# Kernel tuning notes

Hardware: AMD Instinct MI355X
Metric: run time of the kernel (lower is better)

## Reference

```python
import jax, jax.numpy as jnp
import numpy as np

N_NODES = 50000
NEG_SLOPE = 0.2


def gat_conv(x, src, dst, W, a_src, a_dst, bias, heads):
    # x: [N, Fin]; W: [Fin, heads*C]; a_src/a_dst: [heads, C]; bias: [heads*C]
    n = x.shape[0]
    h = (x @ W).reshape(n, heads, -1)              # [N, H, C]
    alpha_src = jnp.einsum('nhc,hc->nh', h, a_src)  # [N, H]
    alpha_dst = jnp.einsum('nhc,hc->nh', h, a_dst)  # [N, H]
    e = alpha_src[src] + alpha_dst[dst]             # [E, H]
    e = jax.nn.leaky_relu(e, NEG_SLOPE)
    # segment softmax over edges grouped by destination node
    m = jax.ops.segment_max(e, dst, num_segments=n)          # [N, H]
    e = jnp.exp(e - jax.lax.stop_gradient(m)[dst])
    s = jax.ops.segment_sum(e, dst, num_segments=n)          # [N, H]
    alpha = e / (s[dst] + 1e-16)                              # [E, H]
    msg = h[src] * alpha[:, :, None]                          # [E, H, C]
    out = jax.ops.segment_sum(msg, dst, num_segments=n)      # [N, H, C]
    return out.reshape(n, -1) + bias


def add_self_loops(edge_index, n):
    loops = jnp.arange(n, dtype=edge_index.dtype)
    src = jnp.concatenate([edge_index[0], loops])
    dst = jnp.concatenate([edge_index[1], loops])
    return src, dst


def setup_inputs() -> dict:
    key = jax.random.key(0)
    ks = jax.random.split(key, 10)
    num_features, num_classes, heads1, c1 = 128, 40, 8, 32
    n_edges = 800000
    x = jax.random.normal(ks[0], (N_NODES, num_features), dtype=jnp.float32)
    edge_index = jax.random.randint(ks[1], (2, n_edges), 0, N_NODES, dtype=jnp.int64)
    sc = 0.1
    W1 = jax.random.normal(ks[2], (num_features, heads1 * c1), dtype=jnp.float32) * sc
    a_src1 = jax.random.normal(ks[3], (heads1, c1), dtype=jnp.float32) * sc
    a_dst1 = jax.random.normal(ks[4], (heads1, c1), dtype=jnp.float32) * sc
    b1 = jnp.zeros((heads1 * c1,), dtype=jnp.float32)
    W2 = jax.random.normal(ks[5], (heads1 * c1, num_classes), dtype=jnp.float32) * sc
    a_src2 = jax.random.normal(ks[6], (1, num_classes), dtype=jnp.float32) * sc
    a_dst2 = jax.random.normal(ks[7], (1, num_classes), dtype=jnp.float32) * sc
    b2 = jnp.zeros((num_classes,), dtype=jnp.float32)
    return {"x": x, "edge_index": edge_index, "W1": W1, "a_src1": a_src1,
            "a_dst1": a_dst1, "b1": b1, "W2": W2, "a_src2": a_src2,
            "a_dst2": a_dst2, "b2": b2}


def reference(x, edge_index, W1, a_src1, a_dst1, b1, W2, a_src2, a_dst2, b2):
    src, dst = add_self_loops(edge_index, x.shape[0])
    h = gat_conv(x, src, dst, W1, a_src1, a_dst1, b1, heads=8)
    h = jax.nn.elu(h)
    h = gat_conv(h, src, dst, W2, a_src2, a_dst2, b2, heads=1)
    return jax.nn.log_softmax(h, axis=1)
```

## Files before the change

### kernel.cpp

```cpp
#include <hip/hip_runtime.h>
#include <math.h>

#define NNODES 50000
#define F_IN   128
#define F1     256
#define H1N    8
#define NCLS   40
#define NEG    0.2f
#define MNEG  -3.0e38f
#define SCAN_BLOCKS 196
#define ACAP   64

typedef unsigned int uint32;
typedef __attribute__((ext_vector_type(8))) short short8v;
typedef __attribute__((ext_vector_type(4))) float f32x4;

__device__ __forceinline__ float leaky(float x) { return x > 0.f ? x : NEG * x; }

__device__ __forceinline__ unsigned short f2bf(float f) {
  uint32 u = __float_as_uint(f);
  u = (u + 0x7FFFu + ((u >> 16) & 1u)) >> 16;
  return (unsigned short)u;
}
__device__ __forceinline__ float bf_lo(uint32 u) { return __uint_as_float(u << 16); }
__device__ __forceinline__ float bf_hi(uint32 u) { return __uint_as_float(u & 0xFFFF0000u); }
__device__ __forceinline__ float bfu(unsigned short u) {
  return __uint_as_float((uint32)u << 16);
}

__global__ __launch_bounds__(256) void convx_k(const float* __restrict__ x,
                                               unsigned short* __restrict__ xb) {
  int i = blockIdx.x * 256 + threadIdx.x;
  float4 v = ((const float4*)x)[i];
  uint2 o;
  o.x = (uint32)f2bf(v.x) | ((uint32)f2bf(v.y) << 16);
  o.y = (uint32)f2bf(v.z) | ((uint32)f2bf(v.w) << 16);
  ((uint2*)xb)[i] = o;
}

__global__ __launch_bounds__(256) void convw_k(const float* __restrict__ W,
                                               unsigned short* __restrict__ Wt) {
  int id = blockIdx.x * 256 + threadIdx.x;
  int k = id >> 8, c = id & 255;
  Wt[c * 128 + k] = f2bf(W[id]);
}

__global__ __launch_bounds__(256) void convw2_k(const float* __restrict__ W2,
                                                unsigned short* __restrict__ Wt2) {
  int id = blockIdx.x * 256 + threadIdx.x;
  int c = id >> 8, k = id & 255;
  Wt2[c * 256 + k] = (c < NCLS) ? f2bf(W2[k * NCLS + c]) : (unsigned short)0;
}

__global__ __launch_bounds__(256) void gemm1_mfma_k(
    const unsigned short* __restrict__ xb, const unsigned short* __restrict__ Wt,
    const float* __restrict__ asrc, const float* __restrict__ adst,
    unsigned short* __restrict__ h1b, float* __restrict__ as1,
    float* __restrict__ ad1) {
  const int lane = threadIdx.x & 63;
  const int wv   = threadIdx.x >> 6;
  const int row0 = blockIdx.x * 64 + wv * 16;
  if (row0 >= NNODES) return;
  const int lrow = lane & 15;
  const int kgrp = lane >> 4;

  const short8v* xp = (const short8v*)xb;
  short8v a[4];
  #pragma unroll
  for (int ks = 0; ks < 4; ++ks)
    a[ks] = xp[(row0 + lrow) * 16 + ks * 4 + kgrp];

  const short8v* wp = (const short8v*)Wt;
  float ps[4] = {0.f, 0.f, 0.f, 0.f};
  float pd[4] = {0.f, 0.f, 0.f, 0.f};

  for (int n = 0; n < 16; ++n) {
    f32x4 acc = {0.f, 0.f, 0.f, 0.f};
    #pragma unroll
    for (int ks = 0; ks < 4; ++ks) {
      short8v b = wp[(n * 16 + lrow) * 16 + ks * 4 + kgrp];
      acc = __builtin_amdgcn_mfma_f32_16x16x32_bf16(a[ks], b, acc, 0, 0, 0);
    }
    const int col = n * 16 + lrow;
    const float ascv = asrc[col];
    const float advv = adst[col];
    #pragma unroll
    for (int r = 0; r < 4; ++r) {
      int row = row0 + kgrp * 4 + r;
      h1b[(long)row * F1 + col] = f2bf(acc[r]);
      ps[r] = fmaf(acc[r], ascv, ps[r]);
      pd[r] = fmaf(acc[r], advv, pd[r]);
    }
    if (n & 1) {
      const int head = n >> 1;
      #pragma unroll
      for (int r = 0; r < 4; ++r) {
        #pragma unroll
        for (int mask = 1; mask <= 8; mask <<= 1) {
          ps[r] += __shfl_xor(ps[r], mask, 64);
          pd[r] += __shfl_xor(pd[r], mask, 64);
        }
      }
      if (lrow == 0) {
        #pragma unroll
        for (int r = 0; r < 4; ++r) {
          int row = row0 + kgrp * 4 + r;
          as1[row * H1N + head] = ps[r];
          ad1[row * H1N + head] = pd[r];
        }
      }
      #pragma unroll
      for (int r = 0; r < 4; ++r) { ps[r] = 0.f; pd[r] = 0.f; }
    }
  }
}

__global__ __launch_bounds__(256) void hist_k(const int* __restrict__ ei,
                                              int* __restrict__ deg, int E, int ET) {
  int e = blockIdx.x * 256 + threadIdx.x;
  if (e >= ET) return;
  int d = (e < E) ? ei[E + e] : e - E;
  atomicAdd(&deg[d], 1);
}

__global__ __launch_bounds__(256) void partsum_k(const int* __restrict__ deg,
                                                 int* __restrict__ blocksum) {
  int idx = blockIdx.x * 256 + threadIdx.x;
  int v = (idx < NNODES) ? deg[idx] : 0;
  #pragma unroll
  for (int m = 32; m >= 1; m >>= 1) v += __shfl_xor(v, m, 64);
  __shared__ int sh[4];
  if ((threadIdx.x & 63) == 0) sh[threadIdx.x >> 6] = v;
  __syncthreads();
  if (threadIdx.x == 0) blocksum[blockIdx.x] = sh[0] + sh[1] + sh[2] + sh[3];
}

__global__ __launch_bounds__(256) void scanblocks_k(const int* __restrict__ blocksum,
                                                    int* __restrict__ blockoff) {
  __shared__ int sh[256];
  int t = threadIdx.x;
  int v = (t < SCAN_BLOCKS) ? blocksum[t] : 0;
  sh[t] = v;
  __syncthreads();
  for (int off = 1; off < 256; off <<= 1) {
    int u = (t >= off) ? sh[t - off] : 0;
    __syncthreads();
    sh[t] += u;
    __syncthreads();
  }
  if (t < SCAN_BLOCKS) blockoff[t] = (t == 0) ? 0 : sh[t - 1];
}

__global__ __launch_bounds__(256) void rowstart_k(const int* __restrict__ deg,
                                                  const int* __restrict__ blockoff,
                                                  int* __restrict__ row_start,
                                                  int* __restrict__ cursor, int ET) {
  __shared__ int sh[256];
  int t = threadIdx.x;
  int idx = blockIdx.x * 256 + t;
  int v = (idx < NNODES) ? deg[idx] : 0;
  sh[t] = v;
  __syncthreads();
  for (int off = 1; off < 256; off <<= 1) {
    int u = (t >= off) ? sh[t - off] : 0;
    __syncthreads();
    sh[t] += u;
    __syncthreads();
  }
  int incl = sh[t];
  int base = blockoff[blockIdx.x];
  if (idx < NNODES) {
    int rs = base + incl - v;
    row_start[idx] = rs;
    cursor[idx] = rs;
    if (idx == NNODES - 1) row_start[NNODES] = base + incl;
  }
}

__global__ __launch_bounds__(256) void scatter_k(const int* __restrict__ ei,
                                                 int* __restrict__ cursor,
                                                 int* __restrict__ csr_src, int E, int ET) {
  int e = blockIdx.x * 256 + threadIdx.x;
  if (e >= ET) return;
  int s, d;
  if (e < E) { s = ei[e]; d = ei[E + e]; } else { s = d = e - E; }
  int pos = atomicAdd(&cursor[d], 1);
  csr_src[pos] = s;
}

__global__ __launch_bounds__(64) void agg1_k(
    const int* __restrict__ row_start, const int* __restrict__ csr_src,
    const float* __restrict__ as1, const float* __restrict__ ad1,
    const uint32* __restrict__ h1b, const float* __restrict__ b1,
    uint32* __restrict__ x2b) {
  __shared__ float alpha_lds[ACAP][H1N];
  __shared__ float rs_lds[8];
  const int d = blockIdx.x;
  const int t = threadIdx.x;
  const int r0 = row_start[d], r1e = row_start[d + 1];

  {
    const int hh = t & 7, slot = t >> 3;
    const float adv = ad1[d * 8 + hh];
    float sum = 0.f;
    for (int i = r0 + slot; i < r1e; i += 8) {
      float ex = __expf(leaky(as1[csr_src[i] * 8 + hh] + adv));
      sum += ex;
      int idx = i - r0;
      if (idx < ACAP) alpha_lds[idx][hh] = ex;
    }
    sum += __shfl_xor(sum, 8, 64);
    sum += __shfl_xor(sum, 16, 64);
    sum += __shfl_xor(sum, 32, 64);
    if (t < 8) rs_lds[t] = 1.f / (sum + 1e-16f);
  }
  __syncthreads();

  const int h = t >> 3;
  const float adh = ad1[d * 8 + h];
  float a0 = 0.f, a1 = 0.f, a2 = 0.f, a3 = 0.f;
  int i = r0;
  for (; i + 2 <= r1e; i += 2) {
    int s0 = csr_src[i], s1 = csr_src[i + 1];
    int i0 = i - r0;
    float w0 = (i0 < ACAP) ? alpha_lds[i0][h]
                           : __expf(leaky(as1[s0 * 8 + h] + adh));
    float w1 = (i0 + 1 < ACAP) ? alpha_lds[i0 + 1][h]
                               : __expf(leaky(as1[s1 * 8 + h] + adh));
    uint2 v0 = ((const uint2*)(h1b + (long)s0 * 128))[t];
    uint2 v1 = ((const uint2*)(h1b + (long)s1 * 128))[t];
    a0 = fmaf(bf_lo(v0.x), w0, a0);
    a1 = fmaf(bf_hi(v0.x), w0, a1);
    a2 = fmaf(bf_lo(v0.y), w0, a2);
    a3 = fmaf(bf_hi(v0.y), w0, a3);
    a0 = fmaf(bf_lo(v1.x), w1, a0);
    a1 = fmaf(bf_hi(v1.x), w1, a1);
    a2 = fmaf(bf_lo(v1.y), w1, a2);
    a3 = fmaf(bf_hi(v1.y), w1, a3);
  }
  if (i < r1e) {
    int s0 = csr_src[i];
    int i0 = i - r0;
    float w0 = (i0 < ACAP) ? alpha_lds[i0][h]
                           : __expf(leaky(as1[s0 * 8 + h] + adh));
    uint2 v0 = ((const uint2*)(h1b + (long)s0 * 128))[t];
    a0 = fmaf(bf_lo(v0.x), w0, a0);
    a1 = fmaf(bf_hi(v0.x), w0, a1);
    a2 = fmaf(bf_lo(v0.y), w0, a2);
    a3 = fmaf(bf_hi(v0.y), w0, a3);
  }
  const float rch = rs_lds[h];
  float4 b = ((const float4*)b1)[t];
  float o0 = a0 * rch + b.x, o1 = a1 * rch + b.y;
  float o2 = a2 * rch + b.z, o3 = a3 * rch + b.w;
  o0 = o0 > 0.f ? o0 : expm1f(o0);
  o1 = o1 > 0.f ? o1 : expm1f(o1);
  o2 = o2 > 0.f ? o2 : expm1f(o2);
  o3 = o3 > 0.f ? o3 : expm1f(o3);
  uint2 o;
  o.x = (uint32)f2bf(o0) | ((uint32)f2bf(o1) << 16);
  o.y = (uint32)f2bf(o2) | ((uint32)f2bf(o3) << 16);
  ((uint2*)(x2b + (long)d * 128))[t] = o;
}

__global__ __launch_bounds__(256) void gemm2_mfma_k(
    const unsigned short* __restrict__ x2b, const unsigned short* __restrict__ Wt2,
    const float* __restrict__ a_src2, const float* __restrict__ a_dst2,
    unsigned short* __restrict__ h2b, float* __restrict__ as2,
    float* __restrict__ ad2) {
  const int lane = threadIdx.x & 63;
  const int wv   = threadIdx.x >> 6;
  const int row0 = blockIdx.x * 64 + wv * 16;
  if (row0 >= NNODES) return;
  const int lrow = lane & 15;
  const int kgrp = lane >> 4;

  const short8v* xp = (const short8v*)x2b;
  short8v a[8];
  #pragma unroll
  for (int ks = 0; ks < 8; ++ks)
    a[ks] = xp[(row0 + lrow) * 32 + ks * 4 + kgrp];

  const short8v* wp = (const short8v*)Wt2;
  float ps[4] = {0.f, 0.f, 0.f, 0.f};
  float pd[4] = {0.f, 0.f, 0.f, 0.f};

  #pragma unroll
  for (int n = 0; n < 3; ++n) {
    f32x4 acc = {0.f, 0.f, 0.f, 0.f};
    #pragma unroll
    for (int ks = 0; ks < 8; ++ks) {
      short8v b = wp[(n * 16 + lrow) * 32 + ks * 4 + kgrp];
      acc = __builtin_amdgcn_mfma_f32_16x16x32_bf16(a[ks], b, acc, 0, 0, 0);
    }
    const int col = n * 16 + lrow;
    const bool valid = col < NCLS;
    const float asv = valid ? a_src2[col] : 0.f;
    const float adv = valid ? a_dst2[col] : 0.f;
    #pragma unroll
    for (int r = 0; r < 4; ++r) {
      int row = row0 + kgrp * 4 + r;
      if (valid) h2b[(long)row * NCLS + col] = f2bf(acc[r]);
      ps[r] = fmaf(acc[r], asv, ps[r]);
      pd[r] = fmaf(acc[r], adv, pd[r]);
    }
  }
  #pragma unroll
  for (int r = 0; r < 4; ++r) {
    #pragma unroll
    for (int mask = 1; mask <= 8; mask <<= 1) {
      ps[r] += __shfl_xor(ps[r], mask, 64);
      pd[r] += __shfl_xor(pd[r], mask, 64);
    }
  }
  if (lrow == 0) {
    #pragma unroll
    for (int r = 0; r < 4; ++r) {
      int row = row0 + kgrp * 4 + r;
      as2[row] = ps[r];
      ad2[row] = pd[r];
    }
  }
}

__global__ __launch_bounds__(256) void agg2_k(
    const int* __restrict__ row_start, const int* __restrict__ csr_src,
    const float* __restrict__ as2, const float* __restrict__ ad2,
    const unsigned short* __restrict__ h2b, const float* __restrict__ b2,
    float* __restrict__ out) {
  __shared__ float acache[4][ACAP];
  int wave = threadIdx.x >> 6, lane = threadIdx.x & 63;
  int d = blockIdx.x * 4 + wave;
  int r0 = row_start[d], r1e = row_start[d + 1];
  const float add = ad2[d];

  float sum = 0.f;
  for (int i = r0 + lane; i < r1e; i += 64) {
    float ex = __expf(leaky(as2[csr_src[i]] + add));
    int idx = i - r0;
    if (idx < ACAP) acache[wave][idx] = ex;
    sum += ex;
  }
  #pragma unroll
  for (int mask = 1; mask <= 32; mask <<= 1) sum += __shfl_xor(sum, mask, 64);
  float rcp = 1.f / (sum + 1e-16f);
  __syncthreads();

  float acc = 0.f;
  int i = r0;
  for (; i + 2 <= r1e; i += 2) {
    int s0 = csr_src[i], s1 = csr_src[i + 1];
    int i0 = i - r0;
    float a0 = (i0 < ACAP) ? acache[wave][i0]
                           : __expf(leaky(as2[s0] + add));
    float a1 = (i0 + 1 < ACAP) ? acache[wave][i0 + 1]
                               : __expf(leaky(as2[s1] + add));
    float v0 = (lane < NCLS) ? bfu(h2b[(long)s0 * NCLS + lane]) : 0.f;
    float v1 = (lane < NCLS) ? bfu(h2b[(long)s1 * NCLS + lane]) : 0.f;
    acc = fmaf(v0, a0, acc);
    acc = fmaf(v1, a1, acc);
  }
  if (i < r1e) {
    int s0 = csr_src[i];
    int i0 = i - r0;
    float a0 = (i0 < ACAP) ? acache[wave][i0]
                           : __expf(leaky(as2[s0] + add));
    float v0 = (lane < NCLS) ? bfu(h2b[(long)s0 * NCLS + lane]) : 0.f;
    acc = fmaf(v0, a0, acc);
  }
  acc *= rcp;

  float v = (lane < NCLS) ? acc + b2[lane] : MNEG;
  float mm = v;
  #pragma unroll
  for (int mask = 1; mask <= 32; mask <<= 1) mm = fmaxf(mm, __shfl_xor(mm, mask, 64));
  float ex = (lane < NCLS) ? __expf(v - mm) : 0.f;
  float se = ex;
  #pragma unroll
  for (int mask = 1; mask <= 32; mask <<= 1) se += __shfl_xor(se, mask, 64);
  if (lane < NCLS) out[(long)d * NCLS + lane] = v - mm - __logf(se);
}

extern "C" void kernel_launch(void* const* d_in, const int* in_sizes, int n_in,
                              void* d_out, int out_size, void* d_ws, size_t ws_size,
                              hipStream_t stream) {
  const float* x      = (const float*)d_in[0];
  const int*   ei     = (const int*)d_in[1];
  const float* W1     = (const float*)d_in[2];
  const float* a_src1 = (const float*)d_in[3];
  const float* a_dst1 = (const float*)d_in[4];
  const float* b1     = (const float*)d_in[5];
  const float* W2     = (const float*)d_in[6];
  const float* a_src2 = (const float*)d_in[7];
  const float* a_dst2 = (const float*)d_in[8];
  const float* b2     = (const float*)d_in[9];
  float* out = (float*)d_out;

  const int E  = in_sizes[1] / 2;
  const int ET = E + NNODES;

  float* ws = (float*)d_ws;
  unsigned short* h1b = (unsigned short*)ws;
  unsigned short* h2b = (unsigned short*)ws;
  float* as2    = ws + 2000000;
  float* ad2    = ws + 2050000;
  uint32* x2b   = (uint32*)(ws + 6400000);
  unsigned short* xb = (unsigned short*)(ws + 9700000);
  unsigned short* Wt = (unsigned short*)(ws + 13000000);
  unsigned short* Wt2 = (unsigned short*)(ws + 13100000);
  float* as1    = ws + 19200000;
  float* ad1    = ws + 19600000;
  int* row_start = (int*)(ws + 26800000);
  int* cursor    = row_start + 50001;
  int* deg       = cursor + 50000;
  int* csr_src   = deg + 50000;
  int* blocksum  = csr_src + 850000;
  int* blockoff  = blocksum + 256;

  hipMemsetAsync(deg, 0, NNODES * sizeof(int), stream);

  hist_k<<<(ET + 255) / 256, 256, 0, stream>>>(ei, deg, E, ET);
  partsum_k<<<SCAN_BLOCKS, 256, 0, stream>>>(deg, blocksum);
  scanblocks_k<<<1, 256, 0, stream>>>(blocksum, blockoff);
  rowstart_k<<<SCAN_BLOCKS, 256, 0, stream>>>(deg, blockoff, row_start, cursor, ET);
  scatter_k<<<(ET + 255) / 256, 256, 0, stream>>>(ei, cursor, csr_src, E, ET);

  convx_k<<<6250, 256, 0, stream>>>(x, xb);
  convw_k<<<128, 256, 0, stream>>>(W1, Wt);
  convw2_k<<<48, 256, 0, stream>>>(W2, Wt2);
  gemm1_mfma_k<<<(NNODES + 63) / 64, 256, 0, stream>>>(xb, Wt, a_src1, a_dst1,
                                                       h1b, as1, ad1);
  agg1_k<<<NNODES, 64, 0, stream>>>(row_start, csr_src, as1, ad1,
                                    (const uint32*)h1b, b1, x2b);

  gemm2_mfma_k<<<(NNODES + 63) / 64, 256, 0, stream>>>(
      (const unsigned short*)x2b, Wt2, a_src2, a_dst2, h2b, as2, ad2);
  agg2_k<<<NNODES / 4, 256, 0, stream>>>(row_start, csr_src, as2, ad2, h2b, b2, out);
}
```

Before: 388.6 us.

## Fuse x bf16 conversion into gemm1 and split agg1 edges across half-waves

Removes the separate convx kernel and converts the fp32 x rows to bf16 inside gemm1's operand load, saving a launch and a round trip of the converted activations through memory. In agg1, each 64-lane wave now splits edges between two 32-lane halves, each lane loading 16-byte chunks of 8 bf16 values, and the halves are combined with a cross-half shuffle before the epilogue. This doubles per-lane memory width and edge-level parallelism, at the cost of extra registers and shuffles, with half the lanes idle during the store.

```diff
diff --git a/kernel.cpp b/kernel.cpp
--- a/kernel.cpp
+++ b/kernel.cpp
@@ -28,16 +28,6 @@
   return __uint_as_float((uint32)u << 16);
 }
 
-__global__ __launch_bounds__(256) void convx_k(const float* __restrict__ x,
-                                               unsigned short* __restrict__ xb) {
-  int i = blockIdx.x * 256 + threadIdx.x;
-  float4 v = ((const float4*)x)[i];
-  uint2 o;
-  o.x = (uint32)f2bf(v.x) | ((uint32)f2bf(v.y) << 16);
-  o.y = (uint32)f2bf(v.z) | ((uint32)f2bf(v.w) << 16);
-  ((uint2*)xb)[i] = o;
-}
-
 __global__ __launch_bounds__(256) void convw_k(const float* __restrict__ W,
                                                unsigned short* __restrict__ Wt) {
   int id = blockIdx.x * 256 + threadIdx.x;
@@ -53,7 +43,7 @@
 }
 
 __global__ __launch_bounds__(256) void gemm1_mfma_k(
-    const unsigned short* __restrict__ xb, const unsigned short* __restrict__ Wt,
+    const float* __restrict__ x, const unsigned short* __restrict__ Wt,
     const float* __restrict__ asrc, const float* __restrict__ adst,
     unsigned short* __restrict__ h1b, float* __restrict__ as1,
     float* __restrict__ ad1) {
@@ -64,11 +54,19 @@
   const int lrow = lane & 15;
   const int kgrp = lane >> 4;
 
-  const short8v* xp = (const short8v*)xb;
+  const float4* xg = (const float4*)(x + (long)(row0 + lrow) * F_IN);
   short8v a[4];
   #pragma unroll
-  for (int ks = 0; ks < 4; ++ks)
-    a[ks] = xp[(row0 + lrow) * 16 + ks * 4 + kgrp];
+  for (int ks = 0; ks < 4; ++ks) {
+    float4 u = xg[ks * 8 + kgrp * 2];
+    float4 v = xg[ks * 8 + kgrp * 2 + 1];
+    short8v t;
+    t[0] = (short)f2bf(u.x); t[1] = (short)f2bf(u.y);
+    t[2] = (short)f2bf(u.z); t[3] = (short)f2bf(u.w);
+    t[4] = (short)f2bf(v.x); t[5] = (short)f2bf(v.y);
+    t[6] = (short)f2bf(v.z); t[7] = (short)f2bf(v.w);
+    a[ks] = t;
+  }
 
   const short8v* wp = (const short8v*)Wt;
   float ps[4] = {0.f, 0.f, 0.f, 0.f};
@@ -216,51 +214,59 @@
   }
   __syncthreads();
 
-  const int h = t >> 3;
+  const int half = t >> 5;
+  const int l = t & 31;
+  const int h = l >> 2;
   const float adh = ad1[d * 8 + h];
   float a0 = 0.f, a1 = 0.f, a2 = 0.f, a3 = 0.f;
-  int i = r0;
-  for (; i + 2 <= r1e; i += 2) {
-    int s0 = csr_src[i], s1 = csr_src[i + 1];
-    int i0 = i - r0;
-    float w0 = (i0 < ACAP) ? alpha_lds[i0][h]
-                           : __expf(leaky(as1[s0 * 8 + h] + adh));
-    float w1 = (i0 + 1 < ACAP) ? alpha_lds[i0 + 1][h]
-                               : __expf(leaky(as1[s1 * 8 + h] + adh));
-    uint2 v0 = ((const uint2*)(h1b + (long)s0 * 128))[t];
-    uint2 v1 = ((const uint2*)(h1b + (long)s1 * 128))[t];
-    a0 = fmaf(bf_lo(v0.x), w0, a0);
-    a1 = fmaf(bf_hi(v0.x), w0, a1);
-    a2 = fmaf(bf_lo(v0.y), w0, a2);
-    a3 = fmaf(bf_hi(v0.y), w0, a3);
-    a0 = fmaf(bf_lo(v1.x), w1, a0);
-    a1 = fmaf(bf_hi(v1.x), w1, a1);
-    a2 = fmaf(bf_lo(v1.y), w1, a2);
-    a3 = fmaf(bf_hi(v1.y), w1, a3);
-  }
-  if (i < r1e) {
+  float a4 = 0.f, a5 = 0.f, a6 = 0.f, a7 = 0.f;
+  for (int i = r0 + half; i < r1e; i += 2) {
     int s0 = csr_src[i];
     int i0 = i - r0;
-    float w0 = (i0 < ACAP) ? alpha_lds[i0][h]
-                           : __expf(leaky(as1[s0 * 8 + h] + adh));
-    uint2 v0 = ((const uint2*)(h1b + (long)s0 * 128))[t];
-    a0 = fmaf(bf_lo(v0.x), w0, a0);
-    a1 = fmaf(bf_hi(v0.x), w0, a1);
-    a2 = fmaf(bf_lo(v0.y), w0, a2);
-    a3 = fmaf(bf_hi(v0.y), w0, a3);
-  }
-  const float rch = rs_lds[h];
-  float4 b = ((const float4*)b1)[t];
-  float o0 = a0 * rch + b.x, o1 = a1 * rch + b.y;
-  float o2 = a2 * rch + b.z, o3 = a3 * rch + b.w;
-  o0 = o0 > 0.f ? o0 : expm1f(o0);
-  o1 = o1 > 0.f ? o1 : expm1f(o1);
-  o2 = o2 > 0.f ? o2 : expm1f(o2);
-  o3 = o3 > 0.f ? o3 : expm1f(o3);
-  uint2 o;
-  o.x = (uint32)f2bf(o0) | ((uint32)f2bf(o1) << 16);
-  o.y = (uint32)f2bf(o2) | ((uint32)f2bf(o3) << 16);
-  ((uint2*)(x2b + (long)d * 128))[t] = o;
+    float w = (i0 < ACAP) ? alpha_lds[i0][h]
+                          : __expf(leaky(as1[s0 * 8 + h] + adh));
+    uint4 v = ((const uint4*)(h1b + (long)s0 * 128))[l];
+    a0 = fmaf(bf_lo(v.x), w, a0);
+    a1 = fmaf(bf_hi(v.x), w, a1);
+    a2 = fmaf(bf_lo(v.y), w, a2);
+    a3 = fmaf(bf_hi(v.y), w, a3);
+    a4 = fmaf(bf_lo(v.z), w, a4);
+    a5 = fmaf(bf_hi(v.z), w, a5);
+    a6 = fmaf(bf_lo(v.w), w, a6);
+    a7 = fmaf(bf_hi(v.w), w, a7);
+  }
+  a0 += __shfl_xor(a0, 32, 64);
+  a1 += __shfl_xor(a1, 32, 64);
+  a2 += __shfl_xor(a2, 32, 64);
+  a3 += __shfl_xor(a3, 32, 64);
+  a4 += __shfl_xor(a4, 32, 64);
+  a5 += __shfl_xor(a5, 32, 64);
+  a6 += __shfl_xor(a6, 32, 64);
+  a7 += __shfl_xor(a7, 32, 64);
+
+  if (half == 0) {
+    const float rch = rs_lds[h];
+    const float4* bp = (const float4*)b1;
+    float4 bA = bp[l * 2], bB = bp[l * 2 + 1];
+    float o0 = a0 * rch + bA.x, o1 = a1 * rch + bA.y;
+    float o2 = a2 * rch + bA.z, o3 = a3 * rch + bA.w;
+    float o4 = a4 * rch + bB.x, o5 = a5 * rch + bB.y;
+    float o6 = a6 * rch + bB.z, o7 = a7 * rch + bB.w;
+    o0 = o0 > 0.f ? o0 : expm1f(o0);
+    o1 = o1 > 0.f ? o1 : expm1f(o1);
+    o2 = o2 > 0.f ? o2 : expm1f(o2);
+    o3 = o3 > 0.f ? o3 : expm1f(o3);
+    o4 = o4 > 0.f ? o4 : expm1f(o4);
+    o5 = o5 > 0.f ? o5 : expm1f(o5);
+    o6 = o6 > 0.f ? o6 : expm1f(o6);
+    o7 = o7 > 0.f ? o7 : expm1f(o7);
+    uint4 o;
+    o.x = (uint32)f2bf(o0) | ((uint32)f2bf(o1) << 16);
+    o.y = (uint32)f2bf(o2) | ((uint32)f2bf(o3) << 16);
+    o.z = (uint32)f2bf(o4) | ((uint32)f2bf(o5) << 16);
+    o.w = (uint32)f2bf(o6) | ((uint32)f2bf(o7) << 16);
+    ((uint4*)(x2b + (long)d * 128))[l] = o;
+  }
 }
 
 __global__ __launch_bounds__(256) void gemm2_mfma_k(
@@ -405,7 +411,6 @@
   float* as2    = ws + 2000000;
   float* ad2    = ws + 2050000;
   uint32* x2b   = (uint32*)(ws + 6400000);
-  unsigned short* xb = (unsigned short*)(ws + 9700000);
   unsigned short* Wt = (unsigned short*)(ws + 13000000);
   unsigned short* Wt2 = (unsigned short*)(ws + 13100000);
   float* as1    = ws + 19200000;
@@ -425,10 +430,9 @@
   rowstart_k<<<SCAN_BLOCKS, 256, 0, stream>>>(deg, blockoff, row_start, cursor, ET);
   scatter_k<<<(ET + 255) / 256, 256, 0, stream>>>(ei, cursor, csr_src, E, ET);
 
-  convx_k<<<6250, 256, 0, stream>>>(x, xb);
   convw_k<<<128, 256, 0, stream>>>(W1, Wt);
   convw2_k<<<48, 256, 0, stream>>>(W2, Wt2);
-  gemm1_mfma_k<<<(NNODES + 63) / 64, 256, 0, stream>>>(xb, Wt, a_src1, a_dst1,
+  gemm1_mfma_k<<<(NNODES + 63) / 64, 256, 0, stream>>>(x, Wt, a_src1, a_dst1,
                                                        h1b, as1, ad1);
   agg1_k<<<NNODES, 64, 0, stream>>>(row_start, csr_src, as1, ad1,
                                     (const uint32*)h1b, b1, x2b);
```

New measurement: 383.9 us. Within noise of the previous version (-1.2%).
